# Kernel optimization log

Measured on AMD Instinct MI355X. Metric: run time of the kernel, lower is better.

Reference implementation:

```python
import jax, jax.numpy as jnp
import numpy as np

B, J, D, T = 4096, 22, 3, 50  # batch, joints, xyz dims, seq_len
N = J * D                     # 66 channels
LW = 3                        # local_window
TAU = 5.0
EPS = 1e-5


def _chain_adj_mask(n):
    m = np.zeros((n, n), dtype=np.float32)
    for i in range(n - 1):
        m[i, i + 1] = 1.0
        m[i + 1, i] = 1.0
    return m


def _band_mask(t, w):
    i = np.arange(t)
    return (np.abs(i[:, None] - i[None, :]) <= w).astype(np.float32)


def setup_inputs() -> dict:
    key = jax.random.key(0)
    ks = jax.random.split(key, 9)
    x = jax.random.normal(ks[0], (B, N, T), dtype=jnp.float32)
    adj = jnp.eye(J, dtype=jnp.float32) + 0.1 * jax.random.normal(ks[1], (J, J), dtype=jnp.float32)
    adj_t = 0.1 * jax.random.normal(ks[2], (T, T), dtype=jnp.float32)
    adj_jc = 0.1 * jax.random.normal(ks[3], (J, D, D), dtype=jnp.float32)
    adj_tj = 0.1 * jax.random.normal(ks[4], (N, T, T), dtype=jnp.float32)
    mlp = jax.random.normal(ks[5], (T, 4), dtype=jnp.float32)
    w_update = 1e-2 * jax.random.normal(ks[6], (T, T), dtype=jnp.float32)
    b_update = jnp.zeros((T,), dtype=jnp.float32)
    alpha = jnp.ones((1, N, 1), dtype=jnp.float32)
    beta = jnp.zeros((1, N, 1), dtype=jnp.float32)
    adj_mask = jnp.asarray(_chain_adj_mask(J))
    traj_mask = jnp.asarray(_band_mask(T, LW))
    u = jax.random.uniform(ks[7], (B, 4), minval=1e-6, maxval=1.0 - 1e-6, dtype=jnp.float32)
    gumbels = -jnp.log(-jnp.log(u))
    return {"x": x, "adj": adj, "adj_t": adj_t, "adj_jc": adj_jc, "adj_tj": adj_tj,
            "mlp": mlp, "w_update": w_update, "b_update": b_update,
            "alpha": alpha, "beta": beta, "adj_mask": adj_mask,
            "traj_mask": traj_mask, "gumbels": gumbels}


def reference(x, adj, adj_t, adj_jc, adj_tj, mlp, w_update, b_update,
              alpha, beta, adj_mask, traj_mask, gumbels):
    xr = x.reshape(B, J, D, T)
    # spatial GC: masked joint-joint adjacency
    x1 = jnp.einsum('vj,bjct->bvct', adj * adj_mask, xr).reshape(B, N, T)
    # temporal GC: banded time-time adjacency shared over channels
    x2 = jnp.einsum('ft,bnt->bnf', adj_t * traj_mask, x)
    # joint-channel GC: per-joint 3x3 channel mixing
    x3 = jnp.einsum('jkc,bjct->bjkt', adj_jc, xr).reshape(B, N, T)
    # spatio-temporal GC: per-channel banded time-time adjacency
    x4 = jnp.einsum('nft,bnt->bnf', adj_tj * traj_mask[None], x)
    # gate: mean-pool over channels -> [B,T] @ [T,4], hard gumbel-softmax
    prob = x.mean(axis=1) @ mlp
    y = jax.nn.softmax((prob + gumbels) / TAU, axis=-1)
    y_hard = jax.nn.one_hot(jnp.argmax(y, axis=-1), 4, dtype=y.dtype)
    gate = y_hard + y - jax.lax.stop_gradient(y)  # straight-through
    # option 0 is zeros, so only options 1..3 contribute
    x_ = (gate[:, 1, None, None] * x2
          + gate[:, 2, None, None] * x3
          + gate[:, 3, None, None] * x4)
    # update linear along time axis
    x_ = (x1 + x_) @ w_update.T + b_update
    # spatial LayerNorm over channel axis
    mean = x_.mean(axis=1, keepdims=True)
    var = ((x_ - mean) ** 2).mean(axis=1, keepdims=True)
    x_ = (x_ - mean) / jnp.sqrt(var + EPS) * alpha + beta
    return x + x_
```

## Files before the change

kernel.cpp:

```cpp
#include <hip/hip_runtime.h>


typedef __attribute__((ext_vector_type(8))) short short8_t;
typedef __attribute__((ext_vector_type(4))) float f32x4_t;

__device__ __forceinline__ unsigned short f2bf(float f) {
    unsigned u = __float_as_uint(f);
    u += 0x7fffu + ((u >> 16) & 1u);
    return (unsigned short)(u >> 16);
}
__device__ __forceinline__ float bf2f(unsigned us) {
    return __uint_as_float(us << 16);
}

#define XLD(nn, tt) (*(const uint2*)((const char*)xbf + (((((nn) << 6) + (tt)) << 1) ^ (((nn) & 7) << 4))))

__global__ __launch_bounds__(256) void pack_kernel(
    const float* __restrict__ adj_t,
    const float* __restrict__ adj_tj,
    unsigned short* __restrict__ ws)
{
    int i = blockIdx.x * 256 + threadIdx.x;
    if (i < 400) {
        int f = i >> 3, j = i & 7;
        int tt = f - 3 + j;
        float v = (j < 7 && tt >= 0 && tt < 50) ? adj_t[f * 50 + tt] : 0.f;
        ws[i] = f2bf(v);
    } else if (i < 26800) {
        int e = i - 400;
        int nf = e >> 3, j = e & 7;
        int f = nf % 50;
        int tt = f - 3 + j;
        float v = (j < 7 && tt >= 0 && tt < 50) ? adj_tj[(size_t)nf * 50 + tt] : 0.f;
        ws[i] = f2bf(v);
    }
}

__global__ __launch_bounds__(256, 2) void dyn_kernel(
    const float* __restrict__ x,
    const float* __restrict__ adj,
    const float* __restrict__ adj_t,
    const float* __restrict__ adj_jc,
    const float* __restrict__ adj_tj,
    const float* __restrict__ mlp,
    const float* __restrict__ w_update,
    const float* __restrict__ alpha,
    const float* __restrict__ beta,
    const float* __restrict__ gumbels,
    const unsigned short* __restrict__ wpack,
    int packed,
    float* __restrict__ out)
{
    __shared__ unsigned short xbf[66 * 64];
    __shared__ float wsum[16];
    __shared__ float as[66], bs[66];

    const int b    = blockIdx.x;
    const int tid  = threadIdx.x;
    const int lane = tid & 63;
    const int wv   = tid >> 6;
    const int li   = lane & 15;
    const int lq   = lane >> 4;
    const int f    = wv * 16 + li;
    const float* __restrict__ xb = x + (size_t)b * 3300;

    const float4 gv = *(const float4*)(gumbels + (size_t)b * 4);

    int sn[4], st0[4], sv[4];
    float cwm[4], cwp[4];
    #pragma unroll
    for (int r = 0; r < 4; ++r) {
        int i = tid + (r << 8);
        if (r == 3 && i > 857) i = 857;
        int n = i / 13, q = i - n * 13;
        sn[r] = n; st0[r] = q * 4;
        int v = n / 3; sv[r] = v;
        cwm[r] = (v > 0)  ? adj[v * 22 + v - 1] : 0.f;
        cwp[r] = (v < 21) ? adj[v * 22 + v + 1] : 0.f;
    }

    short8_t bfrag0, bfrag1;
    #pragma unroll
    for (int j = 0; j < 8; ++j) {
        int k0 = 8 * lq + j;
        int k1 = 32 + 8 * lq + j;
        float v0 = (f < 50) ? w_update[f * 50 + k0] : 0.f;
        float v1 = (f < 50 && k1 < 50) ? w_update[f * 50 + k1] : 0.f;
        bfrag0[j] = (short)f2bf(v0);
        bfrag1[j] = (short)f2bf(v1);
    }

    for (int i = tid; i < 198; i += 256) {
        int n = i / 3, p = i - n * 3;
        int t0 = 52 + p * 4;
        int byteoff = ((n * 64 + t0) * 2) ^ ((n & 7) << 4);
        uint2 z2; z2.x = 0u; z2.y = 0u;
        *(uint2*)((char*)xbf + byteoff) = z2;
    }
    if (tid < 66) { as[tid] = alpha[tid]; bs[tid] = beta[tid]; }

    float2 xa[4], xc[4];
    #pragma unroll
    for (int r = 0; r < 4; ++r) {
        int off = sn[r] * 50 + st0[r];
        xa[r] = *(const float2*)(xb + off);
        int off2 = off + 2; if (off2 > 3298) off2 = 3298;
        xc[r] = *(const float2*)(xb + off2);
    }
    float4 pl = {0.f, 0.f, 0.f, 0.f};
    const float4* __restrict__ mlp4 = (const float4*)mlp;
    #pragma unroll
    for (int r = 0; r < 4; ++r) {
        int n = sn[r], t0 = st0[r];
        bool full = (t0 < 48);
        float v0 = xa[r].x, v1 = xa[r].y;
        float v2 = full ? xc[r].x : 0.f;
        float v3 = full ? xc[r].y : 0.f;
        float4 m0 = mlp4[t0], m1 = mlp4[t0 + 1];
        int i2 = t0 + 2; if (i2 > 49) i2 = 49;
        int i3 = t0 + 3; if (i3 > 49) i3 = 49;
        float4 m2 = mlp4[i2], m3 = mlp4[i3];
        if (r < 3 || tid < 90) {
            pl.x += v0 * m0.x + v1 * m1.x + v2 * m2.x + v3 * m3.x;
            pl.y += v0 * m0.y + v1 * m1.y + v2 * m2.y + v3 * m3.y;
            pl.z += v0 * m0.z + v1 * m1.z + v2 * m2.z + v3 * m3.z;
            pl.w += v0 * m0.w + v1 * m1.w + v2 * m2.w + v3 * m3.w;
        }
        uint2 pk;
        pk.x = (unsigned)f2bf(v0) | ((unsigned)f2bf(v1) << 16);
        pk.y = (unsigned)f2bf(v2) | ((unsigned)f2bf(v3) << 16);
        *(uint2*)((char*)xbf + (((n * 64 + t0) * 2) ^ ((n & 7) << 4))) = pk;
    }
    #pragma unroll
    for (int d = 1; d < 64; d <<= 1) {
        pl.x += __shfl_xor(pl.x, d, 64);
        pl.y += __shfl_xor(pl.y, d, 64);
        pl.z += __shfl_xor(pl.z, d, 64);
        pl.w += __shfl_xor(pl.w, d, 64);
    }
    if (lane == 0) *(float4*)&wsum[wv * 4] = pl;
    __syncthreads();

    int g;
    {
        float4 s0 = *(const float4*)&wsum[0],  s1 = *(const float4*)&wsum[4];
        float4 s2 = *(const float4*)&wsum[8],  s3 = *(const float4*)&wsum[12];
        const float inv = 1.0f / 66.0f;
        float l0 = (s0.x + s1.x + s2.x + s3.x) * inv + gv.x;
        float l1 = (s0.y + s1.y + s2.y + s3.y) * inv + gv.y;
        float l2 = (s0.z + s1.z + s2.z + s3.z) * inv + gv.z;
        float l3 = (s0.w + s1.w + s2.w + s3.w) * inv + gv.w;
        g = 0; float bv = l0;
        if (l1 > bv) { bv = l1; g = 1; }
        if (l2 > bv) { bv = l2; g = 2; }
        if (l3 > bv) { bv = l3; g = 3; }
    }

    uint2 zpk[4];
    if (g == 1 || g == 3) {
        uint4 w0[4], w1[4];
        auto loadrows = [&](int r, uint4* dst) {
            if (packed) {
                const uint4* wt4 = (const uint4*)
                    ((g == 1) ? wpack : wpack + 400 + (size_t)sn[r] * 400);
                #pragma unroll
                for (int k = 0; k < 4; ++k) {
                    int ff = st0[r] + k; if (ff > 49) ff = 49;
                    dst[k] = wt4[ff];
                }
            } else {
                const float* rb = (g == 1) ? adj_t : (adj_tj + (size_t)sn[r] * 2500);
                #pragma unroll
                for (int k = 0; k < 4; ++k) {
                    int ff = st0[r] + k; if (ff > 49) ff = 49;
                    float w[8];
                    #pragma unroll
                    for (int j = 0; j < 8; ++j) {
                        int tt = ff - 3 + j;
                        w[j] = (j < 7 && tt >= 0 && tt < 50) ? rb[ff * 50 + tt] : 0.f;
                    }
                    uint4 u;
                    u.x = (unsigned)f2bf(w[0]) | ((unsigned)f2bf(w[1]) << 16);
                    u.y = (unsigned)f2bf(w[2]) | ((unsigned)f2bf(w[3]) << 16);
                    u.z = (unsigned)f2bf(w[4]) | ((unsigned)f2bf(w[5]) << 16);
                    u.w = (unsigned)f2bf(w[6]) | ((unsigned)f2bf(w[7]) << 16);
                    dst[k] = u;
                }
            }
        };
        loadrows(0, w0);
        #pragma unroll
        for (int r = 0; r < 4; ++r) {
            uint4* wcur = (r & 1) ? w1 : w0;
            uint4* wnxt = (r & 1) ? w0 : w1;
            if (r < 3) loadrows(r + 1, wnxt);
            int n = sn[r], t0 = st0[r];
            uint2 pm = {0u, 0u}, pp = {0u, 0u};
            if (n >= 3)  pm = XLD(n - 3, t0);
            if (n <= 62) pp = XLD(n + 3, t0);
            float acc0 = cwm[r] * bf2f(pm.x & 0xffff) + cwp[r] * bf2f(pp.x & 0xffff);
            float acc1 = cwm[r] * bf2f(pm.x >> 16)    + cwp[r] * bf2f(pp.x >> 16);
            float acc2 = cwm[r] * bf2f(pm.y & 0xffff) + cwp[r] * bf2f(pp.y & 0xffff);
            float acc3 = cwm[r] * bf2f(pm.y >> 16)    + cwp[r] * bf2f(pp.y >> 16);
            float xr[12];
            if (t0 >= 4) {
                uint2 p0 = XLD(n, t0 - 4);
                xr[0] = bf2f(p0.x & 0xffff); xr[1] = bf2f(p0.x >> 16);
                xr[2] = bf2f(p0.y & 0xffff); xr[3] = bf2f(p0.y >> 16);
            } else { xr[0] = 0.f; xr[1] = 0.f; xr[2] = 0.f; xr[3] = 0.f; }
            {
                uint2 p1 = XLD(n, t0);
                xr[4] = bf2f(p1.x & 0xffff); xr[5] = bf2f(p1.x >> 16);
                xr[6] = bf2f(p1.y & 0xffff); xr[7] = bf2f(p1.y >> 16);
            }
            {
                uint2 p2 = XLD(n, t0 + 4);
                xr[8]  = bf2f(p2.x & 0xffff); xr[9]  = bf2f(p2.x >> 16);
                xr[10] = bf2f(p2.y & 0xffff); xr[11] = bf2f(p2.y >> 16);
            }
            #pragma unroll
            for (int j = 0; j < 4; ++j) {
                int ff = t0 + j;
                if (ff < 50) {
                    uint4 u = wcur[j];
                    float a = bf2f(u.x & 0xffff) * xr[j + 1]
                            + bf2f(u.x >> 16)    * xr[j + 2]
                            + bf2f(u.y & 0xffff) * xr[j + 3]
                            + bf2f(u.y >> 16)    * xr[j + 4]
                            + bf2f(u.z & 0xffff) * xr[j + 5]
                            + bf2f(u.z >> 16)    * xr[j + 6]
                            + bf2f(u.w & 0xffff) * xr[j + 7];
                    if (j == 0) acc0 += a; else if (j == 1) acc1 += a;
                    else if (j == 2) acc2 += a; else acc3 += a;
                }
            }
            zpk[r].x = (unsigned)f2bf(acc0) | ((unsigned)f2bf(acc1) << 16);
            zpk[r].y = (unsigned)f2bf(acc2) | ((unsigned)f2bf(acc3) << 16);
        }
    } else {
        #pragma unroll
        for (int r = 0; r < 4; ++r) {
            int n = sn[r], t0 = st0[r], v = sv[r];
            uint2 pm = {0u, 0u}, pp = {0u, 0u};
            if (n >= 3)  pm = XLD(n - 3, t0);
            if (n <= 62) pp = XLD(n + 3, t0);
            float acc0 = cwm[r] * bf2f(pm.x & 0xffff) + cwp[r] * bf2f(pp.x & 0xffff);
            float acc1 = cwm[r] * bf2f(pm.x >> 16)    + cwp[r] * bf2f(pp.x >> 16);
            float acc2 = cwm[r] * bf2f(pm.y & 0xffff) + cwp[r] * bf2f(pp.y & 0xffff);
            float acc3 = cwm[r] * bf2f(pm.y >> 16)    + cwp[r] * bf2f(pp.y >> 16);
            if (g == 2) {
                int c = n - v * 3;
                const float* ajc = adj_jc + (size_t)(v * 3 + c) * 3;
                #pragma unroll
                for (int cc = 0; cc < 3; ++cc) {
                    float w = ajc[cc];
                    uint2 p = XLD(v * 3 + cc, t0);
                    acc0 += w * bf2f(p.x & 0xffff); acc1 += w * bf2f(p.x >> 16);
                    acc2 += w * bf2f(p.y & 0xffff); acc3 += w * bf2f(p.y >> 16);
                }
            }
            zpk[r].x = (unsigned)f2bf(acc0) | ((unsigned)f2bf(acc1) << 16);
            zpk[r].y = (unsigned)f2bf(acc2) | ((unsigned)f2bf(acc3) << 16);
        }
    }
    __syncthreads();

    #pragma unroll
    for (int r = 0; r < 4; ++r) {
        int n = sn[r], t0 = st0[r];
        *(uint2*)((char*)xbf + (((n * 64 + t0) * 2) ^ ((n & 7) << 4))) = zpk[r];
    }
    __syncthreads();

    f32x4_t dacc[5];
    #pragma unroll
    for (int mt = 0; mt < 5; ++mt) dacc[mt] = (f32x4_t){0.f, 0.f, 0.f, 0.f};

    #pragma unroll
    for (int ks = 0; ks < 2; ++ks) {
        short8_t bfrag = ks ? bfrag1 : bfrag0;
        #pragma unroll
        for (int mt = 0; mt < 5; ++mt) {
            int m = mt * 16 + li;
            short8_t afrag = {0, 0, 0, 0, 0, 0, 0, 0};
            if (m < 66)
                afrag = *(const short8_t*)((const char*)xbf + (((m * 64 + 8 * lq + 32 * ks) * 2) ^ ((m & 7) << 4)));
            dacc[mt] = __builtin_amdgcn_mfma_f32_16x16x32_bf16(afrag, bfrag, dacc[mt], 0, 0, 0);
        }
    }

    float S = 0.f, SS = 0.f;
    #pragma unroll
    for (int mt = 0; mt < 5; ++mt) {
        #pragma unroll
        for (int r = 0; r < 4; ++r) {
            int m = mt * 16 + lq * 4 + r;
            if (mt < 4 || m < 66) { float d = dacc[mt][r]; S += d; SS += d * d; }
        }
    }
    S  += __shfl_xor(S, 16, 64);  S  += __shfl_xor(S, 32, 64);
    SS += __shfl_xor(SS, 16, 64); SS += __shfl_xor(SS, 32, 64);
    const float mean = S * (1.f / 66.f);
    const float var  = SS * (1.f / 66.f) - mean * mean;
    const float rstd = rsqrtf(var + 1e-5f);

    if (f < 50) {
        float* __restrict__ ob = out + (size_t)b * 3300;
        #pragma unroll
        for (int mt = 0; mt < 5; ++mt) {
            #pragma unroll
            for (int r = 0; r < 4; ++r) {
                int m = mt * 16 + lq * 4 + r;
                if (mt < 4 || m < 66) {
                    float xv = xb[m * 50 + f];
                    float xn = (dacc[mt][r] - mean) * rstd;
                    ob[m * 50 + f] = xv + xn * as[m] + bs[m];
                }
            }
        }
    }
}

extern "C" void kernel_launch(void* const* d_in, const int* in_sizes, int n_in,
                              void* d_out, int out_size, void* d_ws, size_t ws_size,
                              hipStream_t stream) {
    (void)in_sizes; (void)n_in; (void)out_size;
    const float* x        = (const float*)d_in[0];
    const float* adj      = (const float*)d_in[1];
    const float* adj_t    = (const float*)d_in[2];
    const float* adj_jc   = (const float*)d_in[3];
    const float* adj_tj   = (const float*)d_in[4];
    const float* mlp      = (const float*)d_in[5];
    const float* w_update = (const float*)d_in[6];
    const float* alpha    = (const float*)d_in[8];
    const float* beta     = (const float*)d_in[9];
    const float* gumbels  = (const float*)d_in[12];

    const size_t pack_bytes = (size_t)26800 * sizeof(unsigned short);
    int packed = (d_ws != nullptr && ws_size >= pack_bytes) ? 1 : 0;
    unsigned short* ws = (unsigned short*)d_ws;
    if (packed)
        pack_kernel<<<105, 256, 0, stream>>>(adj_t, adj_tj, ws);

    dyn_kernel<<<4096, 256, 0, stream>>>(x, adj, adj_t, adj_jc, adj_tj, mlp,
                                         w_update, alpha, beta, gumbels,
                                         ws, packed, (float*)d_out);
}
```

Before: 61.33 us.

## Process several batches per block with double-buffered LDS prefetch of next batch

Each block now handles four consecutive batch items, double-buffering the bf16 copy of x and the gate partial sums so the next item's global load and pooling overlap the current item's graph-conv and MFMA work. Per-block setup such as w_update fragments and padding zeroing is amortised across items. The residual add now reads x from the bf16 LDS copy instead of reloading fp32 from global memory, which saves traffic but adds bf16 rounding error to the output. The grid shrinks fourfold, reducing the parallelism available to hide latency.

```diff
diff --git a/kernel.cpp b/kernel.cpp
--- a/kernel.cpp
+++ b/kernel.cpp
@@ -3,6 +3,8 @@
 
 typedef __attribute__((ext_vector_type(8))) short short8_t;
 typedef __attribute__((ext_vector_type(4))) float f32x4_t;
+
+#define CHUNK 4
 
 __device__ __forceinline__ unsigned short f2bf(float f) {
     unsigned u = __float_as_uint(f);
@@ -12,8 +14,12 @@
 __device__ __forceinline__ float bf2f(unsigned us) {
     return __uint_as_float(us << 16);
 }
-
-#define XLD(nn, tt) (*(const uint2*)((const char*)xbf + (((((nn) << 6) + (tt)) << 1) ^ (((nn) & 7) << 4))))
+__device__ __forceinline__ uint2 qld(const unsigned short* base, int n, int t) {
+    return *(const uint2*)((const char*)base + (((n * 64 + t) * 2) ^ ((n & 7) << 4)));
+}
+__device__ __forceinline__ void qst(unsigned short* base, int n, int t, uint2 v) {
+    *(uint2*)((char*)base + (((n * 64 + t) * 2) ^ ((n & 7) << 4))) = v;
+}
 
 __global__ __launch_bounds__(256) void pack_kernel(
     const float* __restrict__ adj_t,
@@ -51,20 +57,18 @@
     int packed,
     float* __restrict__ out)
 {
-    __shared__ unsigned short xbf[66 * 64];
-    __shared__ float wsum[16];
+    __shared__ unsigned short xls[2][66 * 64];
+    __shared__ unsigned short zls[66 * 64];
+    __shared__ float wsum[2][16];
     __shared__ float as[66], bs[66];
 
-    const int b    = blockIdx.x;
     const int tid  = threadIdx.x;
     const int lane = tid & 63;
     const int wv   = tid >> 6;
     const int li   = lane & 15;
     const int lq   = lane >> 4;
     const int f    = wv * 16 + li;
-    const float* __restrict__ xb = x + (size_t)b * 3300;
-
-    const float4 gv = *(const float4*)(gumbels + (size_t)b * 4);
+    const int bbase = blockIdx.x * CHUNK;
 
     int sn[4], st0[4], sv[4];
     float cwm[4], cwp[4];
@@ -93,231 +97,256 @@
     for (int i = tid; i < 198; i += 256) {
         int n = i / 3, p = i - n * 3;
         int t0 = 52 + p * 4;
-        int byteoff = ((n * 64 + t0) * 2) ^ ((n & 7) << 4);
         uint2 z2; z2.x = 0u; z2.y = 0u;
-        *(uint2*)((char*)xbf + byteoff) = z2;
+        qst(xls[0], n, t0, z2);
+        qst(xls[1], n, t0, z2);
+        qst(zls,    n, t0, z2);
     }
     if (tid < 66) { as[tid] = alpha[tid]; bs[tid] = beta[tid]; }
 
     float2 xa[4], xc[4];
+    float4 gvreg[2];
+    const float4* __restrict__ mlp4 = (const float4*)mlp;
+
+    auto stage_load = [&](int bidx) {
+        const float* xbp = x + (size_t)bidx * 3300;
+        #pragma unroll
+        for (int r = 0; r < 4; ++r) {
+            int off = sn[r] * 50 + st0[r];
+            xa[r] = *(const float2*)(xbp + off);
+            int off2 = off + 2; if (off2 > 3298) off2 = 3298;
+            xc[r] = *(const float2*)(xbp + off2);
+        }
+    };
+    auto stage_finish = [&](unsigned short* xd, float* wsd) {
+        float4 pl = {0.f, 0.f, 0.f, 0.f};
+        #pragma unroll
+        for (int r = 0; r < 4; ++r) {
+            int n = sn[r], t0 = st0[r];
+            bool full = (t0 < 48);
+            float v0 = xa[r].x, v1 = xa[r].y;
+            float v2 = full ? xc[r].x : 0.f;
+            float v3 = full ? xc[r].y : 0.f;
+            float4 m0 = mlp4[t0], m1 = mlp4[t0 + 1];
+            int i2 = t0 + 2; if (i2 > 49) i2 = 49;
+            int i3 = t0 + 3; if (i3 > 49) i3 = 49;
+            float4 m2 = mlp4[i2], m3 = mlp4[i3];
+            if (r < 3 || tid < 90) {
+                pl.x += v0 * m0.x + v1 * m1.x + v2 * m2.x + v3 * m3.x;
+                pl.y += v0 * m0.y + v1 * m1.y + v2 * m2.y + v3 * m3.y;
+                pl.z += v0 * m0.z + v1 * m1.z + v2 * m2.z + v3 * m3.z;
+                pl.w += v0 * m0.w + v1 * m1.w + v2 * m2.w + v3 * m3.w;
+            }
+            uint2 pk;
+            pk.x = (unsigned)f2bf(v0) | ((unsigned)f2bf(v1) << 16);
+            pk.y = (unsigned)f2bf(v2) | ((unsigned)f2bf(v3) << 16);
+            qst(xd, n, t0, pk);
+        }
+        #pragma unroll
+        for (int d = 1; d < 64; d <<= 1) {
+            pl.x += __shfl_xor(pl.x, d, 64);
+            pl.y += __shfl_xor(pl.y, d, 64);
+            pl.z += __shfl_xor(pl.z, d, 64);
+            pl.w += __shfl_xor(pl.w, d, 64);
+        }
+        if (lane == 0) *(float4*)wsd = pl;
+    };
+
+    stage_load(bbase);
+    gvreg[0] = *(const float4*)(gumbels + (size_t)bbase * 4);
+    stage_finish(xls[0], &wsum[0][wv * 4]);
+    __syncthreads();
+
     #pragma unroll
-    for (int r = 0; r < 4; ++r) {
-        int off = sn[r] * 50 + st0[r];
-        xa[r] = *(const float2*)(xb + off);
-        int off2 = off + 2; if (off2 > 3298) off2 = 3298;
-        xc[r] = *(const float2*)(xb + off2);
-    }
-    float4 pl = {0.f, 0.f, 0.f, 0.f};
-    const float4* __restrict__ mlp4 = (const float4*)mlp;
-    #pragma unroll
-    for (int r = 0; r < 4; ++r) {
-        int n = sn[r], t0 = st0[r];
-        bool full = (t0 < 48);
-        float v0 = xa[r].x, v1 = xa[r].y;
-        float v2 = full ? xc[r].x : 0.f;
-        float v3 = full ? xc[r].y : 0.f;
-        float4 m0 = mlp4[t0], m1 = mlp4[t0 + 1];
-        int i2 = t0 + 2; if (i2 > 49) i2 = 49;
-        int i3 = t0 + 3; if (i3 > 49) i3 = 49;
-        float4 m2 = mlp4[i2], m3 = mlp4[i3];
-        if (r < 3 || tid < 90) {
-            pl.x += v0 * m0.x + v1 * m1.x + v2 * m2.x + v3 * m3.x;
-            pl.y += v0 * m0.y + v1 * m1.y + v2 * m2.y + v3 * m3.y;
-            pl.z += v0 * m0.z + v1 * m1.z + v2 * m2.z + v3 * m3.z;
-            pl.w += v0 * m0.w + v1 * m1.w + v2 * m2.w + v3 * m3.w;
-        }
-        uint2 pk;
-        pk.x = (unsigned)f2bf(v0) | ((unsigned)f2bf(v1) << 16);
-        pk.y = (unsigned)f2bf(v2) | ((unsigned)f2bf(v3) << 16);
-        *(uint2*)((char*)xbf + (((n * 64 + t0) * 2) ^ ((n & 7) << 4))) = pk;
-    }
-    #pragma unroll
-    for (int d = 1; d < 64; d <<= 1) {
-        pl.x += __shfl_xor(pl.x, d, 64);
-        pl.y += __shfl_xor(pl.y, d, 64);
-        pl.z += __shfl_xor(pl.z, d, 64);
-        pl.w += __shfl_xor(pl.w, d, 64);
-    }
-    if (lane == 0) *(float4*)&wsum[wv * 4] = pl;
-    __syncthreads();
-
-    int g;
-    {
-        float4 s0 = *(const float4*)&wsum[0],  s1 = *(const float4*)&wsum[4];
-        float4 s2 = *(const float4*)&wsum[8],  s3 = *(const float4*)&wsum[12];
-        const float inv = 1.0f / 66.0f;
-        float l0 = (s0.x + s1.x + s2.x + s3.x) * inv + gv.x;
-        float l1 = (s0.y + s1.y + s2.y + s3.y) * inv + gv.y;
-        float l2 = (s0.z + s1.z + s2.z + s3.z) * inv + gv.z;
-        float l3 = (s0.w + s1.w + s2.w + s3.w) * inv + gv.w;
-        g = 0; float bv = l0;
-        if (l1 > bv) { bv = l1; g = 1; }
-        if (l2 > bv) { bv = l2; g = 2; }
-        if (l3 > bv) { bv = l3; g = 3; }
-    }
-
-    uint2 zpk[4];
-    if (g == 1 || g == 3) {
-        uint4 w0[4], w1[4];
-        auto loadrows = [&](int r, uint4* dst) {
-            if (packed) {
-                const uint4* wt4 = (const uint4*)
-                    ((g == 1) ? wpack : wpack + 400 + (size_t)sn[r] * 400);
+    for (int k = 0; k < CHUNK; ++k) {
+        const int cur = k & 1, nxt = cur ^ 1;
+        const unsigned short* xbf = xls[cur];
+
+        if (k + 1 < CHUNK) {
+            stage_load(bbase + k + 1);
+            gvreg[nxt] = *(const float4*)(gumbels + (size_t)(bbase + k + 1) * 4);
+        }
+
+        int g;
+        {
+            float4 s0 = *(const float4*)&wsum[cur][0],  s1 = *(const float4*)&wsum[cur][4];
+            float4 s2 = *(const float4*)&wsum[cur][8],  s3 = *(const float4*)&wsum[cur][12];
+            float4 gvv = gvreg[cur];
+            const float inv = 1.0f / 66.0f;
+            float l0 = (s0.x + s1.x + s2.x + s3.x) * inv + gvv.x;
+            float l1 = (s0.y + s1.y + s2.y + s3.y) * inv + gvv.y;
+            float l2 = (s0.z + s1.z + s2.z + s3.z) * inv + gvv.z;
+            float l3 = (s0.w + s1.w + s2.w + s3.w) * inv + gvv.w;
+            g = 0; float bv = l0;
+            if (l1 > bv) { bv = l1; g = 1; }
+            if (l2 > bv) { bv = l2; g = 2; }
+            if (l3 > bv) { bv = l3; g = 3; }
+        }
+
+        uint2 zpk[4];
+        if (g == 1 || g == 3) {
+            uint4 w0[4], w1[4];
+            auto loadrows = [&](int r, uint4* dst) {
+                if (packed) {
+                    const uint4* wt4 = (const uint4*)
+                        ((g == 1) ? wpack : wpack + 400 + (size_t)sn[r] * 400);
+                    #pragma unroll
+                    for (int kk = 0; kk < 4; ++kk) {
+                        int ff = st0[r] + kk; if (ff > 49) ff = 49;
+                        dst[kk] = wt4[ff];
+                    }
+                } else {
+                    const float* rb = (g == 1) ? adj_t : (adj_tj + (size_t)sn[r] * 2500);
+                    #pragma unroll
+                    for (int kk = 0; kk < 4; ++kk) {
+                        int ff = st0[r] + kk; if (ff > 49) ff = 49;
+                        float w[8];
+                        #pragma unroll
+                        for (int j = 0; j < 8; ++j) {
+                            int tt = ff - 3 + j;
+                            w[j] = (j < 7 && tt >= 0 && tt < 50) ? rb[ff * 50 + tt] : 0.f;
+                        }
+                        uint4 u;
+                        u.x = (unsigned)f2bf(w[0]) | ((unsigned)f2bf(w[1]) << 16);
+                        u.y = (unsigned)f2bf(w[2]) | ((unsigned)f2bf(w[3]) << 16);
+                        u.z = (unsigned)f2bf(w[4]) | ((unsigned)f2bf(w[5]) << 16);
+                        u.w = (unsigned)f2bf(w[6]) | ((unsigned)f2bf(w[7]) << 16);
+                        dst[kk] = u;
+                    }
+                }
+            };
+            loadrows(0, w0);
+            #pragma unroll
+            for (int r = 0; r < 4; ++r) {
+                uint4* wcur = (r & 1) ? w1 : w0;
+                uint4* wnxt = (r & 1) ? w0 : w1;
+                if (r < 3) loadrows(r + 1, wnxt);
+                int n = sn[r], t0 = st0[r];
+                uint2 pm = {0u, 0u}, pp = {0u, 0u};
+                if (n >= 3)  pm = qld(xbf, n - 3, t0);
+                if (n <= 62) pp = qld(xbf, n + 3, t0);
+                float acc0 = cwm[r] * bf2f(pm.x & 0xffff) + cwp[r] * bf2f(pp.x & 0xffff);
+                float acc1 = cwm[r] * bf2f(pm.x >> 16)    + cwp[r] * bf2f(pp.x >> 16);
+                float acc2 = cwm[r] * bf2f(pm.y & 0xffff) + cwp[r] * bf2f(pp.y & 0xffff);
+                float acc3 = cwm[r] * bf2f(pm.y >> 16)    + cwp[r] * bf2f(pp.y >> 16);
+                float xr[12];
+                if (t0 >= 4) {
+                    uint2 p0 = qld(xbf, n, t0 - 4);
+                    xr[0] = bf2f(p0.x & 0xffff); xr[1] = bf2f(p0.x >> 16);
+                    xr[2] = bf2f(p0.y & 0xffff); xr[3] = bf2f(p0.y >> 16);
+                } else { xr[0] = 0.f; xr[1] = 0.f; xr[2] = 0.f; xr[3] = 0.f; }
+                {
+                    uint2 p1 = qld(xbf, n, t0);
+                    xr[4] = bf2f(p1.x & 0xffff); xr[5] = bf2f(p1.x >> 16);
+                    xr[6] = bf2f(p1.y & 0xffff); xr[7] = bf2f(p1.y >> 16);
+                }
+                {
+                    uint2 p2 = qld(xbf, n, t0 + 4);
+                    xr[8]  = bf2f(p2.x & 0xffff); xr[9]  = bf2f(p2.x >> 16);
+                    xr[10] = bf2f(p2.y & 0xffff); xr[11] = bf2f(p2.y >> 16);
+                }
                 #pragma unroll
-                for (int k = 0; k < 4; ++k) {
-                    int ff = st0[r] + k; if (ff > 49) ff = 49;
-                    dst[k] = wt4[ff];
-                }
-            } else {
-                const float* rb = (g == 1) ? adj_t : (adj_tj + (size_t)sn[r] * 2500);
-                #pragma unroll
-                for (int k = 0; k < 4; ++k) {
-                    int ff = st0[r] + k; if (ff > 49) ff = 49;
-                    float w[8];
+                for (int j = 0; j < 4; ++j) {
+                    int ff = t0 + j;
+                    if (ff < 50) {
+                        uint4 u = wcur[j];
+                        float a = bf2f(u.x & 0xffff) * xr[j + 1]
+                                + bf2f(u.x >> 16)    * xr[j + 2]
+                                + bf2f(u.y & 0xffff) * xr[j + 3]
+                                + bf2f(u.y >> 16)    * xr[j + 4]
+                                + bf2f(u.z & 0xffff) * xr[j + 5]
+                                + bf2f(u.z >> 16)    * xr[j + 6]
+                                + bf2f(u.w & 0xffff) * xr[j + 7];
+                        if (j == 0) acc0 += a; else if (j == 1) acc1 += a;
+                        else if (j == 2) acc2 += a; else acc3 += a;
+                    }
+                }
+                zpk[r].x = (unsigned)f2bf(acc0) | ((unsigned)f2bf(acc1) << 16);
+                zpk[r].y = (unsigned)f2bf(acc2) | ((unsigned)f2bf(acc3) << 16);
+            }
+        } else {
+            #pragma unroll
+            for (int r = 0; r < 4; ++r) {
+                int n = sn[r], t0 = st0[r], v = sv[r];
+                uint2 pm = {0u, 0u}, pp = {0u, 0u};
+                if (n >= 3)  pm = qld(xbf, n - 3, t0);
+                if (n <= 62) pp = qld(xbf, n + 3, t0);
+                float acc0 = cwm[r] * bf2f(pm.x & 0xffff) + cwp[r] * bf2f(pp.x & 0xffff);
+                float acc1 = cwm[r] * bf2f(pm.x >> 16)    + cwp[r] * bf2f(pp.x >> 16);
+                float acc2 = cwm[r] * bf2f(pm.y & 0xffff) + cwp[r] * bf2f(pp.y & 0xffff);
+                float acc3 = cwm[r] * bf2f(pm.y >> 16)    + cwp[r] * bf2f(pp.y >> 16);
+                if (g == 2) {
+                    int c = n - v * 3;
+                    const float* ajc = adj_jc + (size_t)(v * 3 + c) * 3;
                     #pragma unroll
-                    for (int j = 0; j < 8; ++j) {
-                        int tt = ff - 3 + j;
-                        w[j] = (j < 7 && tt >= 0 && tt < 50) ? rb[ff * 50 + tt] : 0.f;
-                    }
-                    uint4 u;
-                    u.x = (unsigned)f2bf(w[0]) | ((unsigned)f2bf(w[1]) << 16);
-                    u.y = (unsigned)f2bf(w[2]) | ((unsigned)f2bf(w[3]) << 16);
-                    u.z = (unsigned)f2bf(w[4]) | ((unsigned)f2bf(w[5]) << 16);
-                    u.w = (unsigned)f2bf(w[6]) | ((unsigned)f2bf(w[7]) << 16);
-                    dst[k] = u;
-                }
-            }
-        };
-        loadrows(0, w0);
-        #pragma unroll
-        for (int r = 0; r < 4; ++r) {
-            uint4* wcur = (r & 1) ? w1 : w0;
-            uint4* wnxt = (r & 1) ? w0 : w1;
-            if (r < 3) loadrows(r + 1, wnxt);
-            int n = sn[r], t0 = st0[r];
-            uint2 pm = {0u, 0u}, pp = {0u, 0u};
-            if (n >= 3)  pm = XLD(n - 3, t0);
-            if (n <= 62) pp = XLD(n + 3, t0);
-            float acc0 = cwm[r] * bf2f(pm.x & 0xffff) + cwp[r] * bf2f(pp.x & 0xffff);
-            float acc1 = cwm[r] * bf2f(pm.x >> 16)    + cwp[r] * bf2f(pp.x >> 16);
-            float acc2 = cwm[r] * bf2f(pm.y & 0xffff) + cwp[r] * bf2f(pp.y & 0xffff);
-            float acc3 = cwm[r] * bf2f(pm.y >> 16)    + cwp[r] * bf2f(pp.y >> 16);
-            float xr[12];
-            if (t0 >= 4) {
-                uint2 p0 = XLD(n, t0 - 4);
-                xr[0] = bf2f(p0.x & 0xffff); xr[1] = bf2f(p0.x >> 16);
-                xr[2] = bf2f(p0.y & 0xffff); xr[3] = bf2f(p0.y >> 16);
-            } else { xr[0] = 0.f; xr[1] = 0.f; xr[2] = 0.f; xr[3] = 0.f; }
-            {
-                uint2 p1 = XLD(n, t0);
-                xr[4] = bf2f(p1.x & 0xffff); xr[5] = bf2f(p1.x >> 16);
-                xr[6] = bf2f(p1.y & 0xffff); xr[7] = bf2f(p1.y >> 16);
-            }
-            {
-                uint2 p2 = XLD(n, t0 + 4);
-                xr[8]  = bf2f(p2.x & 0xffff); xr[9]  = bf2f(p2.x >> 16);
-                xr[10] = bf2f(p2.y & 0xffff); xr[11] = bf2f(p2.y >> 16);
-            }
-            #pragma unroll
-            for (int j = 0; j < 4; ++j) {
-                int ff = t0 + j;
-                if (ff < 50) {
-                    uint4 u = wcur[j];
-                    float a = bf2f(u.x & 0xffff) * xr[j + 1]
-                            + bf2f(u.x >> 16)    * xr[j + 2]
-                            + bf2f(u.y & 0xffff) * xr[j + 3]
-                            + bf2f(u.y >> 16)    * xr[j + 4]
-                            + bf2f(u.z & 0xffff) * xr[j + 5]
-                            + bf2f(u.z >> 16)    * xr[j + 6]
-                            + bf2f(u.w & 0xffff) * xr[j + 7];
-                    if (j == 0) acc0 += a; else if (j == 1) acc1 += a;
-                    else if (j == 2) acc2 += a; else acc3 += a;
-                }
-            }
-            zpk[r].x = (unsigned)f2bf(acc0) | ((unsigned)f2bf(acc1) << 16);
-            zpk[r].y = (unsigned)f2bf(acc2) | ((unsigned)f2bf(acc3) << 16);
-        }
-    } else {
-        #pragma unroll
-        for (int r = 0; r < 4; ++r) {
-            int n = sn[r], t0 = st0[r], v = sv[r];
-            uint2 pm = {0u, 0u}, pp = {0u, 0u};
-            if (n >= 3)  pm = XLD(n - 3, t0);
-            if (n <= 62) pp = XLD(n + 3, t0);
-            float acc0 = cwm[r] * bf2f(pm.x & 0xffff) + cwp[r] * bf2f(pp.x & 0xffff);
-            float acc1 = cwm[r] * bf2f(pm.x >> 16)    + cwp[r] * bf2f(pp.x >> 16);
-            float acc2 = cwm[r] * bf2f(pm.y & 0xffff) + cwp[r] * bf2f(pp.y & 0xffff);
-            float acc3 = cwm[r] * bf2f(pm.y >> 16)    + cwp[r] * bf2f(pp.y >> 16);
-            if (g == 2) {
-                int c = n - v * 3;
-                const float* ajc = adj_jc + (size_t)(v * 3 + c) * 3;
-                #pragma unroll
-                for (int cc = 0; cc < 3; ++cc) {
-                    float w = ajc[cc];
-                    uint2 p = XLD(v * 3 + cc, t0);
-                    acc0 += w * bf2f(p.x & 0xffff); acc1 += w * bf2f(p.x >> 16);
-                    acc2 += w * bf2f(p.y & 0xffff); acc3 += w * bf2f(p.y >> 16);
-                }
-            }
-            zpk[r].x = (unsigned)f2bf(acc0) | ((unsigned)f2bf(acc1) << 16);
-            zpk[r].y = (unsigned)f2bf(acc2) | ((unsigned)f2bf(acc3) << 16);
-        }
-    }
-    __syncthreads();
-
-    #pragma unroll
-    for (int r = 0; r < 4; ++r) {
-        int n = sn[r], t0 = st0[r];
-        *(uint2*)((char*)xbf + (((n * 64 + t0) * 2) ^ ((n & 7) << 4))) = zpk[r];
-    }
-    __syncthreads();
-
-    f32x4_t dacc[5];
-    #pragma unroll
-    for (int mt = 0; mt < 5; ++mt) dacc[mt] = (f32x4_t){0.f, 0.f, 0.f, 0.f};
-
-    #pragma unroll
-    for (int ks = 0; ks < 2; ++ks) {
-        short8_t bfrag = ks ? bfrag1 : bfrag0;
-        #pragma unroll
-        for (int mt = 0; mt < 5; ++mt) {
-            int m = mt * 16 + li;
-            short8_t afrag = {0, 0, 0, 0, 0, 0, 0, 0};
-            if (m < 66)
-                afrag = *(const short8_t*)((const char*)xbf + (((m * 64 + 8 * lq + 32 * ks) * 2) ^ ((m & 7) << 4)));
-            dacc[mt] = __builtin_amdgcn_mfma_f32_16x16x32_bf16(afrag, bfrag, dacc[mt], 0, 0, 0);
-        }
-    }
-
-    float S = 0.f, SS = 0.f;
-    #pragma unroll
-    for (int mt = 0; mt < 5; ++mt) {
-        #pragma unroll
-        for (int r = 0; r < 4; ++r) {
-            int m = mt * 16 + lq * 4 + r;
-            if (mt < 4 || m < 66) { float d = dacc[mt][r]; S += d; SS += d * d; }
-        }
-    }
-    S  += __shfl_xor(S, 16, 64);  S  += __shfl_xor(S, 32, 64);
-    SS += __shfl_xor(SS, 16, 64); SS += __shfl_xor(SS, 32, 64);
-    const float mean = S * (1.f / 66.f);
-    const float var  = SS * (1.f / 66.f) - mean * mean;
-    const float rstd = rsqrtf(var + 1e-5f);
-
-    if (f < 50) {
-        float* __restrict__ ob = out + (size_t)b * 3300;
+                    for (int cc = 0; cc < 3; ++cc) {
+                        float w = ajc[cc];
+                        uint2 p = qld(xbf, v * 3 + cc, t0);
+                        acc0 += w * bf2f(p.x & 0xffff); acc1 += w * bf2f(p.x >> 16);
+                        acc2 += w * bf2f(p.y & 0xffff); acc3 += w * bf2f(p.y >> 16);
+                    }
+                }
+                zpk[r].x = (unsigned)f2bf(acc0) | ((unsigned)f2bf(acc1) << 16);
+                zpk[r].y = (unsigned)f2bf(acc2) | ((unsigned)f2bf(acc3) << 16);
+            }
+        }
+        #pragma unroll
+        for (int r = 0; r < 4; ++r) qst(zls, sn[r], st0[r], zpk[r]);
+
+        if (k + 1 < CHUNK) stage_finish(xls[nxt], &wsum[nxt][wv * 4]);
+
+        __syncthreads();
+
+        f32x4_t dacc[5];
+        #pragma unroll
+        for (int mt = 0; mt < 5; ++mt) dacc[mt] = (f32x4_t){0.f, 0.f, 0.f, 0.f};
+        #pragma unroll
+        for (int ks = 0; ks < 2; ++ks) {
+            short8_t bfrag = ks ? bfrag1 : bfrag0;
+            #pragma unroll
+            for (int mt = 0; mt < 5; ++mt) {
+                int m = mt * 16 + li;
+                short8_t afrag = {0, 0, 0, 0, 0, 0, 0, 0};
+                if (m < 66)
+                    afrag = *(const short8_t*)((const char*)zls + (((m * 64 + 8 * lq + 32 * ks) * 2) ^ ((m & 7) << 4)));
+                dacc[mt] = __builtin_amdgcn_mfma_f32_16x16x32_bf16(afrag, bfrag, dacc[mt], 0, 0, 0);
+            }
+        }
+
+        float S = 0.f, SS = 0.f;
         #pragma unroll
         for (int mt = 0; mt < 5; ++mt) {
             #pragma unroll
             for (int r = 0; r < 4; ++r) {
                 int m = mt * 16 + lq * 4 + r;
-                if (mt < 4 || m < 66) {
-                    float xv = xb[m * 50 + f];
-                    float xn = (dacc[mt][r] - mean) * rstd;
-                    ob[m * 50 + f] = xv + xn * as[m] + bs[m];
-                }
-            }
-        }
+                if (mt < 4 || m < 66) { float d = dacc[mt][r]; S += d; SS += d * d; }
+            }
+        }
+        S  += __shfl_xor(S, 16, 64);  S  += __shfl_xor(S, 32, 64);
+        SS += __shfl_xor(SS, 16, 64); SS += __shfl_xor(SS, 32, 64);
+        const float mean = S * (1.f / 66.f);
+        const float var  = SS * (1.f / 66.f) - mean * mean;
+        const float rstd = rsqrtf(var + 1e-5f);
+
+        if (f < 50) {
+            float* __restrict__ ob = out + (size_t)(bbase + k) * 3300;
+            #pragma unroll
+            for (int mt = 0; mt < 5; ++mt) {
+                #pragma unroll
+                for (int r = 0; r < 4; ++r) {
+                    int m = mt * 16 + lq * 4 + r;
+                    if (mt < 4 || m < 66) {
+                        unsigned short xu = *(const unsigned short*)
+                            ((const char*)xbf + (((m * 64 + f) * 2) ^ ((m & 7) << 4)));
+                        float xv = bf2f((unsigned)xu);
+                        float xn = (dacc[mt][r] - mean) * rstd;
+                        ob[m * 50 + f] = xv + xn * as[m] + bs[m];
+                    }
+                }
+            }
+        }
+
+        if (k + 1 < CHUNK) __syncthreads();
     }
 }
 
@@ -342,7 +371,7 @@
     if (packed)
         pack_kernel<<<105, 256, 0, stream>>>(adj_t, adj_tj, ws);
 
-    dyn_kernel<<<4096, 256, 0, stream>>>(x, adj, adj_t, adj_jc, adj_tj, mlp,
-                                         w_update, alpha, beta, gumbels,
-                                         ws, packed, (float*)d_out);
-}
+    dyn_kernel<<<4096 / CHUNK, 256, 0, stream>>>(x, adj, adj_t, adj_jc, adj_tj, mlp,
+                                                 w_update, alpha, beta, gumbels,
+                                                 ws, packed, (float*)d_out);
+}
```

Result: slower. 179.6 us (+192.8%).
